# Kernel optimization log

Measured on AMD Instinct MI355X. Metric: run time of the kernel, lower is better.

The kernel has to match this reference:

```python
import jax, jax.numpy as jnp
import numpy as np

DIM = 1024
HEADS = 16
B, N = 4, 1024

def setup_inputs() -> dict:
    key = jax.random.key(0)
    k1, k2, k3 = jax.random.split(key, 3)
    x = jax.random.normal(k1, (B, N, DIM), dtype=jnp.float32)
    # xavier-uniform-ish init scale
    Wqkv = jax.random.normal(k2, (3 * DIM, DIM), dtype=jnp.float32) * (1.0 / np.sqrt(DIM))
    bqkv = jnp.zeros((3 * DIM,), dtype=jnp.float32)
    W1 = jax.random.normal(k3, (DIM, DIM), dtype=jnp.float32) * (1.0 / np.sqrt(DIM))
    b1 = jnp.zeros((DIM,), dtype=jnp.float32)
    return {"x": x, "Wqkv": Wqkv, "bqkv": bqkv, "W1": W1, "b1": b1}

def reference(x, Wqkv, bqkv, W1, b1):
    b, n, dim = x.shape
    h = HEADS
    d = dim // h
    scale = dim ** (-0.5)  # NOTE: module scales by full dim, not head dim
    qkv = x @ Wqkv.T + bqkv  # [b, n, 3*dim]
    qkv = qkv.reshape(b, n, 3, h, d)
    q = jnp.transpose(qkv[:, :, 0], (0, 2, 1, 3))  # [b, h, n, d]
    k = jnp.transpose(qkv[:, :, 1], (0, 2, 1, 3))
    v = jnp.transpose(qkv[:, :, 2], (0, 2, 1, 3))
    dots = jnp.einsum('bhid,bhjd->bhij', q, k) * scale
    attn = jax.nn.softmax(dots, axis=-1)
    out = jnp.einsum('bhij,bhjd->bhid', attn, v)
    out = jnp.transpose(out, (0, 2, 1, 3)).reshape(b, n, dim)
    out = out @ W1.T + b1
    return out
```

## Files before the change

kernel.cpp:

```cpp
#include <hip/hip_runtime.h>
#include <cmath>

typedef __bf16 bf16;
typedef __bf16 bf16x8 __attribute__((ext_vector_type(8)));
typedef __bf16 bf16x4 __attribute__((ext_vector_type(4)));
typedef float f32x4 __attribute__((ext_vector_type(4)));

#define MFMA16(a, b, c) __builtin_amdgcn_mfma_f32_16x16x32_bf16(a, b, c, 0, 0, 0)

__device__ __forceinline__ void load_lds16(const void* g, void* l) {
    __builtin_amdgcn_global_load_lds(
        (const __attribute__((address_space(1))) void*)g,
        (__attribute__((address_space(3))) void*)l, 16, 0, 0);
}

__device__ __forceinline__ bf16x8 load8(const bf16* p) { return *(const bf16x8*)p; }
__device__ __forceinline__ bf16x8 load8(const float* p) {
    float4 f0 = *(const float4*)p;
    float4 f1 = *(const float4*)(p + 4);
    bf16x8 r;
    r[0] = (bf16)f0.x; r[1] = (bf16)f0.y; r[2] = (bf16)f0.z; r[3] = (bf16)f0.w;
    r[4] = (bf16)f1.x; r[5] = (bf16)f1.y; r[6] = (bf16)f1.z; r[7] = (bf16)f1.w;
    return r;
}

__global__ __launch_bounds__(256) void cvt3(
    const float* __restrict__ s0, bf16* __restrict__ d0, int n0,
    const float* __restrict__ s1, bf16* __restrict__ d1, int n1,
    const float* __restrict__ s2, bf16* __restrict__ d2, int n2)
{
    int i = blockIdx.x * 256 + threadIdx.x;
    const float* s; bf16* d; int base;
    if (i < n0)                { s = s0; d = d0; base = i; }
    else if (i < n0 + n1)      { s = s1; d = d1; base = i - n0; }
    else if (i < n0 + n1 + n2) { s = s2; d = d2; base = i - n0 - n1; }
    else return;
    *(bf16x8*)(d + (size_t)base * 8) = load8(s + (size_t)base * 8);
}

template <int EPI, typename TB, int BN>
__global__ __launch_bounds__(256) void gemm_bt(
    const bf16* __restrict__ A, const TB* __restrict__ Bm,
    const float* __restrict__ bias,
    bf16* __restrict__ qo, bf16* __restrict__ ko, bf16* __restrict__ vto,
    float* __restrict__ C, int M, int N, int K)
{
    constexpr int WN = BN / 2;
    constexpr int JN = WN / 16;
    constexpr int SLOTS = (128 + BN) * 8;

    __shared__ bf16 As[128 * 64];
    __shared__ bf16 Bs[BN * 64];

    const int tid = threadIdx.x;
    const int l   = tid & 63;
    const int w   = tid >> 6;
    const int wm  = w & 1, wn = w >> 1;
    const int l15 = l & 15;
    const int g   = l >> 4;
    const int swz = l15 & 7;
    const int m0  = blockIdx.y * 128;
    const int n0  = blockIdx.x * BN;

    f32x4 acc[4][JN] = {};

    for (int k0 = 0; k0 < K; k0 += 64) {
        __syncthreads();
        #pragma unroll
        for (int it = 0; it < SLOTS / 256; ++it) {
            int s = it * 256 + w * 64 + l;
            if (s < 1024) {
                int row = s >> 3, pc = s & 7;
                int lc  = pc ^ (row & 7);
                load_lds16(A + (size_t)(m0 + row) * K + k0 + lc * 8, &As[s * 8]);
            } else {
                int t = s - 1024;
                int row = t >> 3, pc = t & 7;
                int lc  = pc ^ (row & 7);
                if constexpr (sizeof(TB) == 2) {
                    load_lds16(Bm + (size_t)(n0 + row) * K + k0 + lc * 8, &Bs[t * 8]);
                } else {
                    *(bf16x8*)&Bs[t * 8] = load8(Bm + (size_t)(n0 + row) * K + k0 + lc * 8);
                }
            }
        }
        __syncthreads();
        #pragma unroll
        for (int kk = 0; kk < 64; kk += 32) {
            bf16x8 aF[4], bF[JN];
            #pragma unroll
            for (int i = 0; i < 4; ++i)
                aF[i] = *(const bf16x8*)&As[(wm * 64 + i * 16 + l15) * 64
                                            + ((((kk >> 3) + g) ^ swz) * 8)];
            #pragma unroll
            for (int j = 0; j < JN; ++j)
                bF[j] = *(const bf16x8*)&Bs[(wn * WN + j * 16 + l15) * 64
                                            + ((((kk >> 3) + g) ^ swz) * 8)];
            #pragma unroll
            for (int i = 0; i < 4; ++i)
                #pragma unroll
                for (int j = 0; j < JN; ++j)
                    acc[i][j] = MFMA16(aF[i], bF[j], acc[i][j]);
        }
    }

    #pragma unroll
    for (int j = 0; j < JN; ++j) {
        int gcol = n0 + wn * WN + j * 16 + l15;
        float bv = bias[gcol];
        if (EPI == 0) {
            int which = gcol >> 10;
            int h  = (gcol >> 6) & 15;
            int dd = gcol & 63;
            #pragma unroll
            for (int i = 0; i < 4; ++i) {
                #pragma unroll
                for (int r = 0; r < 4; ++r) {
                    int grow = m0 + wm * 64 + i * 16 + g * 4 + r;
                    int b    = grow >> 10;
                    int npos = grow & 1023;
                    float v  = acc[i][j][r] + bv;
                    size_t bh = (size_t)(b * 16 + h);
                    if (which == 0)
                        qo[(bh * 1024 + npos) * 64 + dd] = (bf16)v;
                    else if (which == 1)
                        ko[(bh * 1024 + npos) * 64 + dd] = (bf16)v;
                    else
                        vto[(bh * 64 + dd) * 1024 + npos] = (bf16)v;
                }
            }
        } else {
            #pragma unroll
            for (int i = 0; i < 4; ++i)
                #pragma unroll
                for (int r = 0; r < 4; ++r) {
                    int grow = m0 + wm * 64 + i * 16 + g * 4 + r;
                    C[(size_t)grow * N + gcol] = acc[i][j][r] + bv;
                }
        }
    }
}

__global__ __launch_bounds__(256, 4) void attn_fused(
    const bf16* __restrict__ qb, const bf16* __restrict__ kb,
    const bf16* __restrict__ vtb, bf16* __restrict__ attn)
{
    __shared__ __align__(16) bf16 Ks[2 * 64 * 64];
    __shared__ __align__(16) bf16 Vts[2 * 64 * 64];
    __shared__ __align__(16) bf16 Ps[4 * 16 * 64];

    const int tid = threadIdx.x;
    const int l   = tid & 63;
    const int w   = tid >> 6;
    const int l15 = l & 15;
    const int g   = l >> 4;
    const int swz = l15 & 7;
    const int bid = blockIdx.x;
    const int bh  = bid & 63;
    const int qc  = bid >> 6;
    const int m0  = qc * 64 + w * 16;

    const bf16* q_bh  = qb  + (size_t)bh * 65536;
    const bf16* k_bh  = kb  + (size_t)bh * 65536;
    const bf16* vt_bh = vtb + (size_t)bh * 65536;

    bf16x8 qf[2];
    #pragma unroll
    for (int kk = 0; kk < 2; ++kk)
        qf[kk] = *(const bf16x8*)(q_bh + (size_t)(m0 + l15) * 64 + kk * 32 + g * 8);

    f32x4 o[4] = {};
    float lsum = 0.f;
    const float C_EXP = 0.04508422f;

    for (int jt = 0; jt < 8; ++jt) {
        const int j0 = jt * 128;
        __syncthreads();
        #pragma unroll
        for (int h = 0; h < 2; ++h)
            #pragma unroll
            for (int it = 0; it < 2; ++it) {
                int s   = it * 256 + tid;
                int row = s >> 3;
                int lc  = (s & 7) ^ (row & 7);
                load_lds16(k_bh + (size_t)(j0 + h * 64 + row) * 64 + lc * 8,
                           &Ks[h * 4096 + s * 8]);
                load_lds16(vt_bh + (size_t)row * 1024 + j0 + h * 64 + lc * 8,
                           &Vts[h * 4096 + s * 8]);
            }
        __syncthreads();

        #pragma unroll
        for (int h = 0; h < 2; ++h) {
            bf16x8 kf[2][4], vf[2][4];
            #pragma unroll
            for (int kk = 0; kk < 2; ++kk)
                #pragma unroll
                for (int js = 0; js < 4; ++js) {
                    int off = h * 4096 + (js * 16 + l15) * 64
                            + (((kk * 4 + g) ^ swz) * 8);
                    kf[kk][js] = *(const bf16x8*)&Ks[off];
                    vf[kk][js] = *(const bf16x8*)&Vts[off];
                }

            f32x4 s4[4] = {};
            #pragma unroll
            for (int kk = 0; kk < 2; ++kk)
                #pragma unroll
                for (int js = 0; js < 4; ++js)
                    s4[js] = MFMA16(kf[kk][js], qf[kk], s4[js]);

            float ls = 0.f;
            #pragma unroll
            for (int js = 0; js < 4; ++js) {
                bf16x4 pk;
                #pragma unroll
                for (int r = 0; r < 4; ++r) {
                    pk[r] = (bf16)exp2f(s4[js][r] * C_EXP);
                    ls += (float)pk[r];
                }
                int cw = (js * 2 + (g >> 1)) ^ swz;
                *(bf16x4*)&Ps[w * 1024 + l15 * 64 + cw * 8 + (g & 1) * 4] = pk;
            }
            lsum += ls;
            __syncthreads();

            #pragma unroll
            for (int kk = 0; kk < 2; ++kk) {
                bf16x8 pf = *(const bf16x8*)&Ps[w * 1024 + l15 * 64
                                                + (((kk * 4 + g) ^ swz) * 8)];
                #pragma unroll
                for (int ns = 0; ns < 4; ++ns)
                    o[ns] = MFMA16(pf, vf[kk][ns], o[ns]);
            }
        }
    }

    float t = lsum;
    t += __shfl_xor(t, 16);
    t += __shfl_xor(t, 32);
    #pragma unroll
    for (int r = 0; r < 4; ++r) {
        float inv = 1.0f / __shfl(t, g * 4 + r);
        int grow = m0 + g * 4 + r;
        size_t obase = ((size_t)(bh >> 4) * 1024 + grow) * 1024 + (bh & 15) * 64;
        #pragma unroll
        for (int ns = 0; ns < 4; ++ns)
            attn[obase + ns * 16 + l15] = (bf16)(o[ns][r] * inv);
    }
}

extern "C" void kernel_launch(void* const* d_in, const int* in_sizes, int n_in,
                              void* d_out, int out_size, void* d_ws, size_t ws_size,
                              hipStream_t stream)
{
    const float* x    = (const float*)d_in[0];
    const float* Wqkv = (const float*)d_in[1];
    const float* bqkv = (const float*)d_in[2];
    const float* W1   = (const float*)d_in[3];
    const float* b1   = (const float*)d_in[4];
    float* out = (float*)d_out;

    const size_t SEG = (size_t)4 * 16 * 1024 * 64;
    bf16* xbf  = (bf16*)d_ws;
    bf16* qb   = xbf + SEG;
    bf16* kb   = qb + SEG;
    bf16* vtb  = kb + SEG;
    bf16* attnb = xbf;
    bf16* wqkvbf = vtb + SEG;
    bf16* w1bf   = wqkvbf + 3145728;

    const bool cw = ws_size >= (size_t)(5 * SEG) * sizeof(bf16);

    const int nx = 524288;
    const int nw = cw ? 393216 : 0;
    const int n1 = cw ? 131072 : 0;
    const int tot = nx + nw + n1;
    cvt3<<<dim3((tot + 255) / 256), 256, 0, stream>>>(
        x, xbf, nx, Wqkv, wqkvbf, nw, W1, w1bf, n1);

    if (cw)
        gemm_bt<0, bf16, 128><<<dim3(24, 32), 256, 0, stream>>>(
            xbf, wqkvbf, bqkv, qb, kb, vtb, nullptr, 4096, 3072, 1024);
    else
        gemm_bt<0, float, 128><<<dim3(24, 32), 256, 0, stream>>>(
            xbf, Wqkv, bqkv, qb, kb, vtb, nullptr, 4096, 3072, 1024);

    attn_fused<<<dim3(1024), 256, 0, stream>>>(qb, kb, vtb, attnb);

    if (cw)
        gemm_bt<1, bf16, 64><<<dim3(16, 32), 256, 0, stream>>>(
            attnb, w1bf, b1, nullptr, nullptr, nullptr, out, 4096, 1024, 1024);
    else
        gemm_bt<1, float, 64><<<dim3(16, 32), 256, 0, stream>>>(
            attnb, W1, b1, nullptr, nullptr, nullptr, out, 4096, 1024, 1024);
}
```

Measured before the change: 175.5 us.

## Split attention keys across warps and reduce partial outputs through LDS

Each warp in the attention kernel now handles all 64 queries of the block but only a 16-key slice of each key tile, instead of 16 queries against every key. This cuts the per-warp LDS reads of K and V^T and removes one barrier per half-tile. The partial outputs and row sums are then reduced across warps through a reused shared buffer, and each thread writes vectorised bf16 output. In exchange there is more register state, launch bounds lowered from 4 to 3 blocks per SM, and a serialized multi-barrier cross-warp reduction epilogue.

```diff
diff --git a/kernel.cpp b/kernel.cpp
--- a/kernel.cpp
+++ b/kernel.cpp
@@ -141,13 +141,16 @@
     }
 }
 
-__global__ __launch_bounds__(256, 4) void attn_fused(
+__global__ __launch_bounds__(256, 3) void attn_fused(
     const bf16* __restrict__ qb, const bf16* __restrict__ kb,
     const bf16* __restrict__ vtb, bf16* __restrict__ attn)
 {
-    __shared__ __align__(16) bf16 Ks[2 * 64 * 64];
-    __shared__ __align__(16) bf16 Vts[2 * 64 * 64];
-    __shared__ __align__(16) bf16 Ps[4 * 16 * 64];
+    __shared__ __align__(16) char smem[49152];
+    bf16* Ks   = (bf16*)smem;
+    bf16* Vts  = (bf16*)(smem + 16384);
+    bf16* Psm  = (bf16*)(smem + 32768);
+    float* Osum = (float*)smem;
+    float* Dsum = (float*)(smem + 17408);
 
     const int tid = threadIdx.x;
     const int l   = tid & 63;
@@ -158,24 +161,26 @@
     const int bid = blockIdx.x;
     const int bh  = bid & 63;
     const int qc  = bid >> 6;
-    const int m0  = qc * 64 + w * 16;
+    const int m0  = qc * 64;
 
     const bf16* q_bh  = qb  + (size_t)bh * 65536;
     const bf16* k_bh  = kb  + (size_t)bh * 65536;
     const bf16* vt_bh = vtb + (size_t)bh * 65536;
 
-    bf16x8 qf[2];
+    bf16x8 qf[4][2];
     #pragma unroll
-    for (int kk = 0; kk < 2; ++kk)
-        qf[kk] = *(const bf16x8*)(q_bh + (size_t)(m0 + l15) * 64 + kk * 32 + g * 8);
-
-    f32x4 o[4] = {};
-    float lsum = 0.f;
+    for (int qg = 0; qg < 4; ++qg)
+        #pragma unroll
+        for (int ks = 0; ks < 2; ++ks)
+            qf[qg][ks] = *(const bf16x8*)(q_bh
+                + (size_t)(m0 + qg * 16 + l15) * 64 + ks * 32 + g * 8);
+
+    f32x4 o[4][4] = {};
+    float lsum[4] = {};
     const float C_EXP = 0.04508422f;
 
     for (int jt = 0; jt < 8; ++jt) {
         const int j0 = jt * 128;
-        __syncthreads();
         #pragma unroll
         for (int h = 0; h < 2; ++h)
             #pragma unroll
@@ -190,63 +195,102 @@
             }
         __syncthreads();
 
+        bf16x8 vf[4];
+        #pragma unroll
+        for (int ns = 0; ns < 4; ++ns)
+            vf[ns] = *(const bf16x8*)&Vts[(g >> 1) * 4096
+                + (ns * 16 + l15) * 64 + (((w * 2 + (g & 1)) ^ swz) * 8)];
+
         #pragma unroll
         for (int h = 0; h < 2; ++h) {
-            bf16x8 kf[2][4], vf[2][4];
-            #pragma unroll
-            for (int kk = 0; kk < 2; ++kk)
-                #pragma unroll
-                for (int js = 0; js < 4; ++js) {
-                    int off = h * 4096 + (js * 16 + l15) * 64
-                            + (((kk * 4 + g) ^ swz) * 8);
-                    kf[kk][js] = *(const bf16x8*)&Ks[off];
-                    vf[kk][js] = *(const bf16x8*)&Vts[off];
-                }
-
+            const int krow = h * 4096 + (w * 16 + l15) * 64;
+            bf16x8 kf0 = *(const bf16x8*)&Ks[krow + ((g ^ swz) * 8)];
+            bf16x8 kf1 = *(const bf16x8*)&Ks[krow + (((4 + g) ^ swz) * 8)];
             f32x4 s4[4] = {};
             #pragma unroll
-            for (int kk = 0; kk < 2; ++kk)
-                #pragma unroll
-                for (int js = 0; js < 4; ++js)
-                    s4[js] = MFMA16(kf[kk][js], qf[kk], s4[js]);
-
-            float ls = 0.f;
-            #pragma unroll
-            for (int js = 0; js < 4; ++js) {
+            for (int qg = 0; qg < 4; ++qg) {
+                s4[qg] = MFMA16(kf0, qf[qg][0], s4[qg]);
+                s4[qg] = MFMA16(kf1, qf[qg][1], s4[qg]);
+            }
+            #pragma unroll
+            for (int qg = 0; qg < 4; ++qg) {
                 bf16x4 pk;
+                float ls = 0.f;
                 #pragma unroll
                 for (int r = 0; r < 4; ++r) {
-                    pk[r] = (bf16)exp2f(s4[js][r] * C_EXP);
+                    pk[r] = (bf16)exp2f(s4[qg][r] * C_EXP);
                     ls += (float)pk[r];
                 }
-                int cw = (js * 2 + (g >> 1)) ^ swz;
-                *(bf16x4*)&Ps[w * 1024 + l15 * 64 + cw * 8 + (g & 1) * 4] = pk;
-            }
-            lsum += ls;
-            __syncthreads();
-
-            #pragma unroll
-            for (int kk = 0; kk < 2; ++kk) {
-                bf16x8 pf = *(const bf16x8*)&Ps[w * 1024 + l15 * 64
-                                                + (((kk * 4 + g) ^ swz) * 8)];
-                #pragma unroll
-                for (int ns = 0; ns < 4; ++ns)
-                    o[ns] = MFMA16(pf, vf[kk][ns], o[ns]);
-            }
-        }
-    }
-
-    float t = lsum;
-    t += __shfl_xor(t, 16);
-    t += __shfl_xor(t, 32);
+                lsum[qg] += ls;
+                *(bf16x4*)&Psm[w * 2048 + (qg * 16 + l15) * 32 + h * 16 + g * 4] = pk;
+            }
+        }
+        __syncthreads();
+
+        #pragma unroll
+        for (int qg = 0; qg < 4; ++qg) {
+            bf16x8 pf = *(const bf16x8*)&Psm[w * 2048 + (qg * 16 + l15) * 32 + g * 8];
+            #pragma unroll
+            for (int ns = 0; ns < 4; ++ns)
+                o[qg][ns] = MFMA16(pf, vf[ns], o[qg][ns]);
+        }
+    }
+
+    __syncthreads();
+
+    float tq[4];
     #pragma unroll
-    for (int r = 0; r < 4; ++r) {
-        float inv = 1.0f / __shfl(t, g * 4 + r);
-        int grow = m0 + g * 4 + r;
-        size_t obase = ((size_t)(bh >> 4) * 1024 + grow) * 1024 + (bh & 15) * 64;
-        #pragma unroll
-        for (int ns = 0; ns < 4; ++ns)
-            attn[obase + ns * 16 + l15] = (bf16)(o[ns][r] * inv);
+    for (int qg = 0; qg < 4; ++qg) {
+        float t = lsum[qg];
+        t += __shfl_xor(t, 16);
+        t += __shfl_xor(t, 32);
+        tq[qg] = t;
+    }
+    if (g == 0) {
+        #pragma unroll
+        for (int qg = 0; qg < 4; ++qg)
+            Dsum[w * 64 + qg * 16 + l15] = tq[qg];
+    }
+
+    if (w == 0) {
+        #pragma unroll
+        for (int qg = 0; qg < 4; ++qg)
+            #pragma unroll
+            for (int ns = 0; ns < 4; ++ns)
+                *(f32x4*)&Osum[(ns * 16 + l15) * 68 + qg * 16 + g * 4] = o[qg][ns];
+    }
+    __syncthreads();
+    #pragma unroll
+    for (int k = 1; k < 4; ++k) {
+        if (w == k) {
+            #pragma unroll
+            for (int qg = 0; qg < 4; ++qg)
+                #pragma unroll
+                for (int ns = 0; ns < 4; ++ns) {
+                    float* p = &Osum[(ns * 16 + l15) * 68 + qg * 16 + g * 4];
+                    f32x4 t = *(f32x4*)p;
+                    t += o[qg][ns];
+                    *(f32x4*)p = t;
+                }
+        }
+        __syncthreads();
+    }
+
+    {
+        int q   = tid >> 2;
+        int ds0 = (tid & 3) * 16;
+        float inv = 1.0f / (Dsum[q] + Dsum[64 + q] + Dsum[128 + q] + Dsum[192 + q]);
+        bf16x8 o0, o1;
+        #pragma unroll
+        for (int j = 0; j < 8; ++j)
+            o0[j] = (bf16)(Osum[(ds0 + j) * 68 + q] * inv);
+        #pragma unroll
+        for (int j = 0; j < 8; ++j)
+            o1[j] = (bf16)(Osum[(ds0 + 8 + j) * 68 + q] * inv);
+        size_t obase = ((size_t)(bh >> 4) * 1024 + m0 + q) * 1024
+                     + (bh & 15) * 64 + ds0;
+        *(bf16x8*)(attn + obase) = o0;
+        *(bf16x8*)(attn + obase + 8) = o1;
     }
 }
 
```

Result: slower. 180.0 us (+2.6%).
